# Kernel optimization log

Measured on AMD Instinct MI355X. Metric: run time of the kernel, lower is better.

The kernel has to match this reference:

```python
import jax, jax.numpy as jnp
import numpy as np

B, S, D, H = 2, 2048, 1024, 16
HD = D // H  # 64


def setup_inputs() -> dict:
    key = jax.random.key(0)
    ks = jax.random.split(key, 10)
    q = jax.random.normal(ks[0], (B, S, D), dtype=jnp.float32)
    k = jax.random.normal(ks[1], (B, S, D), dtype=jnp.float32)
    v = jax.random.normal(ks[2], (B, S, D), dtype=jnp.float32)
    # additive mask: 1 where attention is disallowed (causal), broadcast over B,H
    mask = (1.0 - jnp.tril(jnp.ones((S, S), dtype=jnp.float32)))[None, None, :, :]
    sc = 1.0 / np.sqrt(D)
    Wk = jax.random.normal(ks[3], (D, D), dtype=jnp.float32) * sc
    bk = jnp.zeros((D,), dtype=jnp.float32)
    Wv = jax.random.normal(ks[4], (D, D), dtype=jnp.float32) * sc
    bv = jnp.zeros((D,), dtype=jnp.float32)
    Wo = jax.random.normal(ks[5], (D, D), dtype=jnp.float32) * sc
    bo = jnp.zeros((D,), dtype=jnp.float32)
    return {"q": q, "k": k, "v": v, "mask": mask,
            "Wk": Wk, "bk": bk, "Wv": Wv, "bv": bv, "Wo": Wo, "bo": bo}


def _split_heads(x):
    b, s, d = x.shape
    return x.reshape(b, s, H, HD).transpose(0, 2, 1, 3)  # [B,H,S,HD]


def reference(q, k, v, mask, Wk, bk, Wv, bv, Wo, bo):
    # NOTE: source bug reproduced — q is projected with Wk (wq is unused).
    _q = _split_heads(q @ Wk + bk)
    _k = _split_heads(k @ Wk + bk)
    _v = _split_heads(v @ Wv + bv)
    scale = jnp.sqrt(jnp.float32(HD)) + 1e-8
    score = jnp.einsum('bhqd,bhkd->bhqk', _q, _k) / scale
    score = score + mask * (-1e9)
    attn = jax.nn.softmax(score, axis=-1)
    o = jnp.einsum('bhqk,bhkd->bhqd', attn, _v)
    o = o.transpose(0, 2, 1, 3).reshape(q.shape[0], q.shape[1], -1)  # [B,S,D]
    # dropout is identity at inference (training=False)
    return o @ Wo + bo
```

## Files before the change

### kernel.cpp

```cpp
#include <hip/hip_runtime.h>


#define Bn 2
#define Sn 2048
#define Dn 1024
#define Hn 16
#define HDn 64

typedef short bs8 __attribute__((ext_vector_type(8)));
typedef short s4v __attribute__((ext_vector_type(4)));
typedef float f32x4 __attribute__((ext_vector_type(4)));
typedef unsigned int u32;
typedef unsigned int u32x4 __attribute__((ext_vector_type(4)));

__device__ __forceinline__ short f2bf(float f) {
    u32 x = __builtin_bit_cast(u32, f);
    x = x + 0x7fffu + ((x >> 16) & 1u);
    return (short)(x >> 16);
}
__device__ __forceinline__ u32 packbf2(float lo, float hi) {
    u32 a = __builtin_bit_cast(u32, lo);
    u32 b = __builtin_bit_cast(u32, hi);
    a = a + 0x7fffu + ((a >> 16) & 1u);
    b = b + 0x7fffu + ((b >> 16) & 1u);
    return (a >> 16) | (b & 0xffff0000u);
}
__device__ __forceinline__ void gload16(const void* g, void* l) {
    __builtin_amdgcn_global_load_lds(
        (const __attribute__((address_space(1))) u32*)g,
        (__attribute__((address_space(3))) u32*)l, 16, 0, 0);
}

__global__ __launch_bounds__(256) void cvt_qkv(const float* __restrict__ q,
                                               const float* __restrict__ k,
                                               const float* __restrict__ v,
                                               short* __restrict__ out) {
    int z = blockIdx.y;
    const float* in = z == 0 ? q : z == 1 ? k : v;
    short* o = out + (size_t)z * (Bn * Sn * Dn);
    int i = blockIdx.x * 256 + threadIdx.x;
    const f32x4* p = reinterpret_cast<const f32x4*>(in) + (size_t)i * 2;
    f32x4 a = p[0], b = p[1];
    bs8 ov;
    ov[0]=f2bf(a[0]); ov[1]=f2bf(a[1]); ov[2]=f2bf(a[2]); ov[3]=f2bf(a[3]);
    ov[4]=f2bf(b[0]); ov[5]=f2bf(b[1]); ov[6]=f2bf(b[2]); ov[7]=f2bf(b[3]);
    reinterpret_cast<bs8*>(o)[i] = ov;
}

__global__ __launch_bounds__(256) void cvt_w(const float* __restrict__ Wk,
                                             const float* __restrict__ Wv,
                                             const float* __restrict__ Wo,
                                             short* __restrict__ Wt) {
    __shared__ float tile[32][33];
    int z = blockIdx.z;
    const float* W = z == 0 ? Wk : z == 1 ? Wv : Wo;
    short* o = Wt + (size_t)z * Dn * Dn;
    int tx = threadIdx.x & 31;
    int ty = threadIdx.x >> 5;
    int bi = blockIdx.y * 32;
    int bo = blockIdx.x * 32;
    #pragma unroll
    for (int k2 = 0; k2 < 4; k2++)
        tile[ty + k2*8][tx] = W[(size_t)(bi + ty + k2*8) * Dn + bo + tx];
    __syncthreads();
    #pragma unroll
    for (int k2 = 0; k2 < 4; k2++)
        o[(size_t)(bo + ty + k2*8) * Dn + bi + tx] = f2bf(tile[tx][ty + k2*8]);
}

template<int MODE>
__global__ __launch_bounds__(256) void gemm_bt(const short* __restrict__ A,
                                               const short* __restrict__ Bt,
                                               const float* __restrict__ bias,
                                               void* __restrict__ Cout) {
    constexpr int K = Dn, N = Dn;
    __shared__ __align__(16) short As[64][32];
    __shared__ __align__(16) short Bs[128][32];
    int tid = threadIdx.x;
    int m0 = blockIdx.x * 64, n0 = blockIdx.y * 128;
    int w = tid >> 6, lane = tid & 63;
    int wr = (w >> 1) * 32, wc = (w & 1) * 64;
    int fr = lane & 15, fq = lane >> 4;
    f32x4 acc[2][4] = {};
    int srow = tid >> 2, scol = (tid & 3) * 8;
    const short* Ag  = A  + (size_t)(m0 + srow) * K + scol;
    const short* Bg0 = Bt + (size_t)(n0 + srow) * K + scol;
    const short* Bg1 = Bt + (size_t)(n0 + 64 + srow) * K + scol;
    short* AsL  = &As[0][0] + tid * 8;
    short* BsL0 = &Bs[0][0] + tid * 8;
    short* BsL1 = &Bs[0][0] + 2048 + tid * 8;

    for (int k0 = 0; k0 < K; k0 += 32) {
        gload16(Ag + k0, AsL);
        gload16(Bg0 + k0, BsL0);
        gload16(Bg1 + k0, BsL1);
        __syncthreads();
        bs8 af[2], bfv[4];
        #pragma unroll
        for (int i = 0; i < 2; i++)
            af[i] = *reinterpret_cast<const bs8*>(&As[wr + i*16 + fr][fq*8]);
        #pragma unroll
        for (int j = 0; j < 4; j++)
            bfv[j] = *reinterpret_cast<const bs8*>(&Bs[wc + j*16 + fr][fq*8]);
        #pragma unroll
        for (int i = 0; i < 2; i++)
            #pragma unroll
            for (int j = 0; j < 4; j++)
                acc[i][j] = __builtin_amdgcn_mfma_f32_16x16x32_bf16(af[i], bfv[j], acc[i][j], 0, 0, 0);
        __syncthreads();
    }

    #pragma unroll
    for (int j = 0; j < 4; j++) {
        int col = n0 + wc + j*16 + fr;
        float bv = bias[col];
        #pragma unroll
        for (int i = 0; i < 2; i++) {
            int row0 = m0 + wr + i*16 + fq*4;
            #pragma unroll
            for (int r = 0; r < 4; r++) {
                float vv = acc[i][j][r] + bv;
                if (MODE == 0) {
                    ((short*)Cout)[(size_t)(row0 + r) * N + col] = f2bf(vv);
                } else if (MODE == 1) {
                    int t = row0 + r, bb = t >> 11, s = t & (Sn - 1);
                    ((short*)Cout)[(size_t)bb * (Dn*Sn) + (size_t)col * Sn + s] = f2bf(vv);
                } else {
                    ((float*)Cout)[(size_t)(row0 + r) * N + col] = vv;
                }
            }
        }
    }
}

__global__ __launch_bounds__(256) void attn_fwd(const short* __restrict__ Qp,
                                                const short* __restrict__ Kp,
                                                const short* __restrict__ Vt,
                                                short* __restrict__ O) {
    __shared__ __align__(16) char Kb[64 * 128];
    __shared__ __align__(16) char Vb[64 * 128];
    __shared__ __align__(16) short Ot[4][16][72];
    int bh = blockIdx.y, bb = bh >> 4, h = bh & 15;
    int tid = threadIdx.x, w = tid >> 6, lane = tid & 63;
    int fr = lane & 15, fq = lane >> 4;
    int hiA = (fq >> 1) & 1;
    int wloc = w * 16 + fr;
    const float C1 = 0.18033688011112042f;

    int sr = tid >> 2;
    int scB = (tid & 3) * 32;
    int swz = (sr & 7) << 4;
    int wofs0 = sr * 128 + (scB ^ swz);
    int wofs1 = sr * 128 + ((scB + 16) ^ swz);
    const short* Kg = Kp + (size_t)(bb * Sn + sr) * Dn + h * HDn + (tid & 3) * 16;
    const short* Vg = Vt + (size_t)bb * (Dn * Sn) + (size_t)(h * HDn + sr) * Sn + (tid & 3) * 16;

    for (int hf = 0; hf < 2; hf++) {
        int qt = hf ? (31 - (int)blockIdx.x) : (int)blockIdx.x;
        int q0 = qt * 64 + w * 16;
        const short* Qg = Qp + (size_t)(bb * Sn + q0 + fr) * Dn + h * HDn + fq * 8;
        bs8 qf0 = *reinterpret_cast<const bs8*>(Qg);
        bs8 qf1 = *reinterpret_cast<const bs8*>(Qg + 32);
        f32x4 oacc[4] = {};
        float m_run = -3e38f, l_run = 0.f;

        for (int kt = 0; kt <= qt; kt++) {
            int kv0 = kt * 64;
            bs8 k0v = *reinterpret_cast<const bs8*>(Kg + (size_t)kv0 * Dn);
            bs8 k1v = *reinterpret_cast<const bs8*>(Kg + (size_t)kv0 * Dn + 8);
            bs8 v0v = *reinterpret_cast<const bs8*>(Vg + kv0);
            bs8 v1v = *reinterpret_cast<const bs8*>(Vg + kv0 + 8);
            __syncthreads();
            *reinterpret_cast<bs8*>(Kb + wofs0) = k0v;
            *reinterpret_cast<bs8*>(Kb + wofs1) = k1v;
            *reinterpret_cast<bs8*>(Vb + wofs0) = v0v;
            *reinterpret_cast<bs8*>(Vb + wofs1) = v1v;
            __syncthreads();

            float p[4][4];
            #pragma unroll
            for (int n = 0; n < 4; n++) {
                int row = n * 16 + fr;
                int rs = (row & 7) << 4;
                bs8 kf0 = *reinterpret_cast<const bs8*>(Kb + row * 128 + ((fq * 16) ^ rs));
                bs8 kf1 = *reinterpret_cast<const bs8*>(Kb + row * 128 + ((64 + fq * 16) ^ rs));
                f32x4 t = {};
                t = __builtin_amdgcn_mfma_f32_16x16x32_bf16(kf0, qf0, t, 0, 0, 0);
                t = __builtin_amdgcn_mfma_f32_16x16x32_bf16(kf1, qf1, t, 0, 0, 0);
                #pragma unroll
                for (int r = 0; r < 4; r++) p[n][r] = t[r] * C1;
            }
            if (kt == qt) {
                #pragma unroll
                for (int n = 0; n < 4; n++)
                    #pragma unroll
                    for (int r = 0; r < 4; r++)
                        if (n * 16 + fq * 4 + r > wloc) p[n][r] = -2e8f;
            }

            float mloc = p[0][0];
            #pragma unroll
            for (int n = 0; n < 4; n++)
                #pragma unroll
                for (int r = 0; r < 4; r++) mloc = fmaxf(mloc, p[n][r]);
            mloc = fmaxf(mloc, __shfl_xor(mloc, 16));
            mloc = fmaxf(mloc, __shfl_xor(mloc, 32));
            float mn = fmaxf(m_run, mloc);
            float fac = exp2f(m_run - mn);
            m_run = mn;
            float ssum = 0.f;
            #pragma unroll
            for (int n = 0; n < 4; n++)
                #pragma unroll
                for (int r = 0; r < 4; r++) {
                    float e = exp2f(p[n][r] - mn);
                    p[n][r] = e; ssum += e;
                }
            ssum += __shfl_xor(ssum, 16);
            ssum += __shfl_xor(ssum, 32);
            l_run = l_run * fac + ssum;
            #pragma unroll
            for (int n = 0; n < 4; n++) oacc[n] *= fac;

            u32 W0 = packbf2(p[0][0], p[0][1]), W1 = packbf2(p[0][2], p[0][3]);
            u32 W2 = packbf2(p[1][0], p[1][1]), W3 = packbf2(p[1][2], p[1][3]);
            u32 W4 = packbf2(p[2][0], p[2][1]), W5 = packbf2(p[2][2], p[2][3]);
            u32 W6 = packbf2(p[3][0], p[3][1]), W7 = packbf2(p[3][2], p[3][3]);
            u32 sA0 = hiA ? W2 : W0, sA1 = hiA ? W3 : W1;
            u32 sA2 = hiA ? W6 : W4, sA3 = hiA ? W7 : W5;
            u32 sB0 = hiA ? W0 : W2, sB1 = hiA ? W1 : W3;
            u32 sB2 = hiA ? W4 : W6, sB3 = hiA ? W5 : W7;
            u32 x16_0 = (u32)__shfl_xor((int)sA0, 16), x16_1 = (u32)__shfl_xor((int)sA1, 16);
            u32 x16_2 = (u32)__shfl_xor((int)sA2, 16), x16_3 = (u32)__shfl_xor((int)sA3, 16);
            u32 x32_0 = (u32)__shfl_xor((int)sB0, 32), x32_1 = (u32)__shfl_xor((int)sB1, 32);
            u32 x32_2 = (u32)__shfl_xor((int)sB2, 32), x32_3 = (u32)__shfl_xor((int)sB3, 32);
            u32 x48_0 = (u32)__shfl_xor((int)sB0, 48), x48_1 = (u32)__shfl_xor((int)sB1, 48);
            u32 x48_2 = (u32)__shfl_xor((int)sB2, 48), x48_3 = (u32)__shfl_xor((int)sB3, 48);
            u32x4 F0, F1;
            F0[0] = fq==0 ? W0   : fq==1 ? x48_0 : fq==2 ? x32_0 : x16_0;
            F0[1] = fq==0 ? W1   : fq==1 ? x48_1 : fq==2 ? x32_1 : x16_1;
            F0[2] = fq==0 ? x16_0 : fq==1 ? x32_0 : fq==2 ? x48_0 : W2;
            F0[3] = fq==0 ? x16_1 : fq==1 ? x32_1 : fq==2 ? x48_1 : W3;
            F1[0] = fq==0 ? W4   : fq==1 ? x48_2 : fq==2 ? x32_2 : x16_2;
            F1[1] = fq==0 ? W5   : fq==1 ? x48_3 : fq==2 ? x32_3 : x16_3;
            F1[2] = fq==0 ? x16_2 : fq==1 ? x32_2 : fq==2 ? x48_2 : W6;
            F1[3] = fq==0 ? x16_3 : fq==1 ? x32_3 : fq==2 ? x48_3 : W7;
            bs8 pf0 = __builtin_bit_cast(bs8, F0);
            bs8 pf1 = __builtin_bit_cast(bs8, F1);

            #pragma unroll
            for (int n = 0; n < 4; n++) {
                int row = n * 16 + fr;
                int rs = (row & 7) << 4;
                bs8 vf0 = *reinterpret_cast<const bs8*>(Vb + row * 128 + ((fq * 16) ^ rs));
                bs8 vf1 = *reinterpret_cast<const bs8*>(Vb + row * 128 + ((64 + fq * 16) ^ rs));
                oacc[n] = __builtin_amdgcn_mfma_f32_16x16x32_bf16(vf0, pf0, oacc[n], 0, 0, 0);
                oacc[n] = __builtin_amdgcn_mfma_f32_16x16x32_bf16(vf1, pf1, oacc[n], 0, 0, 0);
            }
        }

        float inv = 1.f / l_run;
        #pragma unroll
        for (int n = 0; n < 4; n++) {
            s4v ov;
            #pragma unroll
            for (int r = 0; r < 4; r++) ov[r] = f2bf(oacc[n][r] * inv);
            *reinterpret_cast<s4v*>(&Ot[w][fr][n * 16 + fq * 4]) = ov;
        }
        bs8 o0 = *reinterpret_cast<const bs8*>(&Ot[w][fr][fq * 16]);
        bs8 o1 = *reinterpret_cast<const bs8*>(&Ot[w][fr][fq * 16 + 8]);
        short* Og = O + (size_t)(bb * Sn + q0 + fr) * Dn + h * HDn + fq * 16;
        *reinterpret_cast<bs8*>(Og) = o0;
        *reinterpret_cast<bs8*>(Og + 8) = o1;
    }
}

extern "C" void kernel_launch(void* const* d_in, const int* in_sizes, int n_in,
                              void* d_out, int out_size, void* d_ws, size_t ws_size,
                              hipStream_t stream) {
    const float* q  = (const float*)d_in[0];
    const float* k  = (const float*)d_in[1];
    const float* v  = (const float*)d_in[2];
    const float* Wk = (const float*)d_in[4];
    const float* bk = (const float*)d_in[5];
    const float* Wv = (const float*)d_in[6];
    const float* bv = (const float*)d_in[7];
    const float* Wo = (const float*)d_in[8];
    const float* bo = (const float*)d_in[9];

    char* ws = (char*)d_ws;
    const size_t MB = (size_t)1 << 20;
    short* Wall = (short*)ws;
    short* Wkt  = Wall;
    short* Wvt  = Wall + (1 << 20);
    short* Wot  = Wall + 2 * (1 << 20);
    short* qb   = (short*)(ws + 6*MB);
    short* kb   = (short*)(ws + 14*MB);
    short* vb   = (short*)(ws + 22*MB);
    short* Qp   = (short*)(ws + 30*MB);
    short* Kp   = (short*)(ws + 38*MB);
    short* Vtp  = qb;
    short* Oa   = kb;

    cvt_qkv<<<dim3(2048, 3), dim3(256), 0, stream>>>(q, k, v, qb);
    cvt_w<<<dim3(32, 32, 3), dim3(256), 0, stream>>>(Wk, Wv, Wo, Wall);

    dim3 gg(64, 8);
    gemm_bt<0><<<gg, dim3(256), 0, stream>>>(qb, Wkt, bk, Qp);
    gemm_bt<0><<<gg, dim3(256), 0, stream>>>(kb, Wkt, bk, Kp);
    gemm_bt<1><<<gg, dim3(256), 0, stream>>>(vb, Wvt, bv, Vtp);

    attn_fwd<<<dim3(16, 32), dim3(256), 0, stream>>>(Qp, Kp, Vtp, Oa);

    gemm_bt<2><<<gg, dim3(256), 0, stream>>>(Oa, Wot, bo, d_out);
}
```

Measured before the change: 261.1 us.

## Fuse QKV projections into one launch and restructure attention softmax and P exchange

Replaces three projection GEMM launches with one batched 128x128-tile kernel. The score scale is folded into the Q projection epilogue, and V^T is stored with packed hardware bf16 conversions. Attention now runs one query tile per block on a 32x32 grid instead of pairing tiles, so the grid is larger but the load is less balanced. The P operand is exchanged through LDS instead of many cross-lane shuffles, the max-rescale is skipped lazily unless the max grows by more than 8, and the l reduction is deferred to the end. Together these cut launch overhead, VALU and shuffle work, at the cost of extra LDS traffic and a wider tile that may lower occupancy.

```diff
diff --git a/kernel.cpp b/kernel.cpp
--- a/kernel.cpp
+++ b/kernel.cpp
@@ -8,22 +8,19 @@
 #define HDn 64
 
 typedef short bs8 __attribute__((ext_vector_type(8)));
-typedef short s4v __attribute__((ext_vector_type(4)));
 typedef float f32x4 __attribute__((ext_vector_type(4)));
 typedef unsigned int u32;
-typedef unsigned int u32x4 __attribute__((ext_vector_type(4)));
+typedef unsigned int u32x2 __attribute__((ext_vector_type(2)));
 
 __device__ __forceinline__ short f2bf(float f) {
     u32 x = __builtin_bit_cast(u32, f);
     x = x + 0x7fffu + ((x >> 16) & 1u);
     return (short)(x >> 16);
 }
-__device__ __forceinline__ u32 packbf2(float lo, float hi) {
-    u32 a = __builtin_bit_cast(u32, lo);
-    u32 b = __builtin_bit_cast(u32, hi);
-    a = a + 0x7fffu + ((a >> 16) & 1u);
-    b = b + 0x7fffu + ((b >> 16) & 1u);
-    return (a >> 16) | (b & 0xffff0000u);
+__device__ __forceinline__ u32 cvtpk(float lo, float hi) {
+    u32 r;
+    asm("v_cvt_pk_bf16_f32 %0, %1, %2" : "=v"(r) : "v"(lo), "v"(hi));
+    return r;
 }
 __device__ __forceinline__ void gload16(const void* g, void* l) {
     __builtin_amdgcn_global_load_lds(
@@ -68,11 +65,94 @@
         o[(size_t)(bo + ty + k2*8) * Dn + bi + tx] = f2bf(tile[tx][ty + k2*8]);
 }
 
-template<int MODE>
-__global__ __launch_bounds__(256) void gemm_bt(const short* __restrict__ A,
-                                               const short* __restrict__ Bt,
-                                               const float* __restrict__ bias,
-                                               void* __restrict__ Cout) {
+__global__ __launch_bounds__(256) void proj3(const short* __restrict__ qb,
+                                             const short* __restrict__ kb,
+                                             const short* __restrict__ vb,
+                                             const short* __restrict__ Wall,
+                                             const float* __restrict__ bk,
+                                             const float* __restrict__ bv,
+                                             short* __restrict__ Qp,
+                                             short* __restrict__ Kp,
+                                             short* __restrict__ Vtp) {
+    constexpr int K = Dn;
+    __shared__ __align__(16) short As[128 * 32];
+    __shared__ __align__(16) short Bs[128 * 32];
+    int z = blockIdx.z;
+    const short* A  = z == 0 ? qb : z == 1 ? kb : vb;
+    const short* Bt = z == 2 ? Wall + (1 << 20) : Wall;
+    const float* bias = z == 2 ? bv : bk;
+    int tid = threadIdx.x;
+    int m0 = blockIdx.x * 128, n0 = blockIdx.y * 128;
+    int w = tid >> 6, lane = tid & 63;
+    int wr = (w >> 1) * 64, wc = (w & 1) * 64;
+    int fr = lane & 15, fq = lane >> 4;
+    f32x4 acc[4][4] = {};
+    const short* Ag  = A  + (size_t)(m0 + (tid >> 2)) * K + (tid & 3) * 8;
+    const short* Ag2 = Ag + (size_t)64 * K;
+    const short* Bg  = Bt + (size_t)(n0 + (tid >> 2)) * K + (tid & 3) * 8;
+    const short* Bg2 = Bg + (size_t)64 * K;
+    short* AsL = As + tid * 8;
+    short* BsL = Bs + tid * 8;
+
+    for (int k0 = 0; k0 < K; k0 += 32) {
+        gload16(Ag + k0, AsL);
+        gload16(Ag2 + k0, AsL + 2048);
+        gload16(Bg + k0, BsL);
+        gload16(Bg2 + k0, BsL + 2048);
+        __syncthreads();
+        bs8 af[4], bfv[4];
+        #pragma unroll
+        for (int i = 0; i < 4; i++)
+            af[i] = *reinterpret_cast<const bs8*>(&As[(wr + i*16 + fr) * 32 + fq * 8]);
+        #pragma unroll
+        for (int j = 0; j < 4; j++)
+            bfv[j] = *reinterpret_cast<const bs8*>(&Bs[(wc + j*16 + fr) * 32 + fq * 8]);
+        #pragma unroll
+        for (int i = 0; i < 4; i++)
+            #pragma unroll
+            for (int j = 0; j < 4; j++)
+                acc[i][j] = __builtin_amdgcn_mfma_f32_16x16x32_bf16(af[i], bfv[j], acc[i][j], 0, 0, 0);
+        __syncthreads();
+    }
+
+    if (z == 2) {
+        #pragma unroll
+        for (int j = 0; j < 4; j++) {
+            int col = n0 + wc + j*16 + fr;
+            float bvv = bias[col];
+            #pragma unroll
+            for (int i = 0; i < 4; i++) {
+                int row0 = m0 + wr + i*16 + fq*4;
+                int bb = row0 >> 11, s0 = row0 & (Sn - 1);
+                size_t base = (size_t)bb * (Dn * Sn) + (size_t)col * Sn + s0;
+                u32x2 pv;
+                pv[0] = cvtpk(acc[i][j][0] + bvv, acc[i][j][1] + bvv);
+                pv[1] = cvtpk(acc[i][j][2] + bvv, acc[i][j][3] + bvv);
+                *reinterpret_cast<u32x2*>(&Vtp[base]) = pv;
+            }
+        }
+    } else {
+        float sc = (z == 0) ? 0.18033688011112042f : 1.0f;
+        short* outp = (z == 0) ? Qp : Kp;
+        #pragma unroll
+        for (int j = 0; j < 4; j++) {
+            int col = n0 + wc + j*16 + fr;
+            float bvv = bias[col];
+            #pragma unroll
+            for (int i = 0; i < 4; i++) {
+                int row0 = m0 + wr + i*16 + fq*4;
+                #pragma unroll
+                for (int r = 0; r < 4; r++)
+                    outp[(size_t)(row0 + r) * Dn + col] = f2bf((acc[i][j][r] + bvv) * sc);
+            }
+        }
+    }
+}
+
+__global__ __launch_bounds__(256) void gemm_out(const short* __restrict__ A,
+                                                const short* __restrict__ Bt,
+                                                const float* __restrict__ bias,
+                                                float* __restrict__ Cout) {
     constexpr int K = Dn, N = Dn;
     __shared__ __align__(16) short As[64][32];
     __shared__ __align__(16) short Bs[128][32];
@@ -82,13 +162,12 @@
     int wr = (w >> 1) * 32, wc = (w & 1) * 64;
     int fr = lane & 15, fq = lane >> 4;
     f32x4 acc[2][4] = {};
-    int srow = tid >> 2, scol = (tid & 3) * 8;
-    const short* Ag  = A  + (size_t)(m0 + srow) * K + scol;
-    const short* Bg0 = Bt + (size_t)(n0 + srow) * K + scol;
-    const short* Bg1 = Bt + (size_t)(n0 + 64 + srow) * K + scol;
+    const short* Ag  = A  + (size_t)(m0 + (tid >> 2)) * K + (tid & 3) * 8;
+    const short* Bg0 = Bt + (size_t)(n0 + (tid >> 2)) * K + (tid & 3) * 8;
+    const short* Bg1 = Bg0 + (size_t)64 * K;
     short* AsL  = &As[0][0] + tid * 8;
     short* BsL0 = &Bs[0][0] + tid * 8;
-    short* BsL1 = &Bs[0][0] + 2048 + tid * 8;
+    short* BsL1 = BsL0 + 2048;
 
     for (int k0 = 0; k0 < K; k0 += 32) {
         gload16(Ag + k0, AsL);
@@ -109,7 +188,6 @@
                 acc[i][j] = __builtin_amdgcn_mfma_f32_16x16x32_bf16(af[i], bfv[j], acc[i][j], 0, 0, 0);
         __syncthreads();
     }
-
     #pragma unroll
     for (int j = 0; j < 4; j++) {
         int col = n0 + wc + j*16 + fr;
@@ -118,17 +196,8 @@
         for (int i = 0; i < 2; i++) {
             int row0 = m0 + wr + i*16 + fq*4;
             #pragma unroll
-            for (int r = 0; r < 4; r++) {
-                float vv = acc[i][j][r] + bv;
-                if (MODE == 0) {
-                    ((short*)Cout)[(size_t)(row0 + r) * N + col] = f2bf(vv);
-                } else if (MODE == 1) {
-                    int t = row0 + r, bb = t >> 11, s = t & (Sn - 1);
-                    ((short*)Cout)[(size_t)bb * (Dn*Sn) + (size_t)col * Sn + s] = f2bf(vv);
-                } else {
-                    ((float*)Cout)[(size_t)(row0 + r) * N + col] = vv;
-                }
-            }
+            for (int r = 0; r < 4; r++)
+                Cout[(size_t)(row0 + r) * N + col] = acc[i][j][r] + bv;
         }
     }
 }
@@ -139,140 +208,127 @@
                                                 short* __restrict__ O) {
     __shared__ __align__(16) char Kb[64 * 128];
     __shared__ __align__(16) char Vb[64 * 128];
+    __shared__ __align__(16) u32  Pw[4][16][36];
     __shared__ __align__(16) short Ot[4][16][72];
+    int qt = 31 - (int)blockIdx.x;
     int bh = blockIdx.y, bb = bh >> 4, h = bh & 15;
     int tid = threadIdx.x, w = tid >> 6, lane = tid & 63;
     int fr = lane & 15, fq = lane >> 4;
-    int hiA = (fq >> 1) & 1;
     int wloc = w * 16 + fr;
-    const float C1 = 0.18033688011112042f;
-
-    int sr = tid >> 2;
-    int scB = (tid & 3) * 32;
-    int swz = (sr & 7) << 4;
+    int q0 = qt * 64 + w * 16;
+
+    const short* Qg = Qp + (size_t)(bb * Sn + q0 + fr) * Dn + h * HDn + fq * 8;
+    bs8 qf0 = *reinterpret_cast<const bs8*>(Qg);
+    bs8 qf1 = *reinterpret_cast<const bs8*>(Qg + 32);
+
+    f32x4 oacc[4] = {};
+    float m_run = -3e38f, l_run = 0.f;
+
+    int sr = tid >> 2, scB = (tid & 3) * 32, swz = (sr & 7) << 4;
     int wofs0 = sr * 128 + (scB ^ swz);
     int wofs1 = sr * 128 + ((scB + 16) ^ swz);
     const short* Kg = Kp + (size_t)(bb * Sn + sr) * Dn + h * HDn + (tid & 3) * 16;
     const short* Vg = Vt + (size_t)bb * (Dn * Sn) + (size_t)(h * HDn + sr) * Sn + (tid & 3) * 16;
 
-    for (int hf = 0; hf < 2; hf++) {
-        int qt = hf ? (31 - (int)blockIdx.x) : (int)blockIdx.x;
-        int q0 = qt * 64 + w * 16;
-        const short* Qg = Qp + (size_t)(bb * Sn + q0 + fr) * Dn + h * HDn + fq * 8;
-        bs8 qf0 = *reinterpret_cast<const bs8*>(Qg);
-        bs8 qf1 = *reinterpret_cast<const bs8*>(Qg + 32);
-        f32x4 oacc[4] = {};
-        float m_run = -3e38f, l_run = 0.f;
-
-        for (int kt = 0; kt <= qt; kt++) {
-            int kv0 = kt * 64;
-            bs8 k0v = *reinterpret_cast<const bs8*>(Kg + (size_t)kv0 * Dn);
-            bs8 k1v = *reinterpret_cast<const bs8*>(Kg + (size_t)kv0 * Dn + 8);
-            bs8 v0v = *reinterpret_cast<const bs8*>(Vg + kv0);
-            bs8 v1v = *reinterpret_cast<const bs8*>(Vg + kv0 + 8);
-            __syncthreads();
-            *reinterpret_cast<bs8*>(Kb + wofs0) = k0v;
-            *reinterpret_cast<bs8*>(Kb + wofs1) = k1v;
-            *reinterpret_cast<bs8*>(Vb + wofs0) = v0v;
-            *reinterpret_cast<bs8*>(Vb + wofs1) = v1v;
-            __syncthreads();
-
-            float p[4][4];
-            #pragma unroll
-            for (int n = 0; n < 4; n++) {
-                int row = n * 16 + fr;
-                int rs = (row & 7) << 4;
-                bs8 kf0 = *reinterpret_cast<const bs8*>(Kb + row * 128 + ((fq * 16) ^ rs));
-                bs8 kf1 = *reinterpret_cast<const bs8*>(Kb + row * 128 + ((64 + fq * 16) ^ rs));
-                f32x4 t = {};
-                t = __builtin_amdgcn_mfma_f32_16x16x32_bf16(kf0, qf0, t, 0, 0, 0);
-                t = __builtin_amdgcn_mfma_f32_16x16x32_bf16(kf1, qf1, t, 0, 0, 0);
-                #pragma unroll
-                for (int r = 0; r < 4; r++) p[n][r] = t[r] * C1;
-            }
-            if (kt == qt) {
-                #pragma unroll
-                for (int n = 0; n < 4; n++)
-                    #pragma unroll
-                    for (int r = 0; r < 4; r++)
-                        if (n * 16 + fq * 4 + r > wloc) p[n][r] = -2e8f;
-            }
-
-            float mloc = p[0][0];
+    int rs = (fr & 7) << 4;
+    int rb0 = (fq * 16) ^ rs;
+    int rb1 = (64 + fq * 16) ^ rs;
+    u32* PwL = &Pw[w][fr][0];
+    u32* PwS = PwL + 2 * fq;
+
+    for (int kt = 0; kt <= qt; kt++) {
+        int kv0 = kt * 64;
+        bs8 k0v = *reinterpret_cast<const bs8*>(Kg + (size_t)kv0 * Dn);
+        bs8 k1v = *reinterpret_cast<const bs8*>(Kg + (size_t)kv0 * Dn + 8);
+        bs8 v0v = *reinterpret_cast<const bs8*>(Vg + kv0);
+        bs8 v1v = *reinterpret_cast<const bs8*>(Vg + kv0 + 8);
+        __syncthreads();
+        *reinterpret_cast<bs8*>(Kb + wofs0) = k0v;
+        *reinterpret_cast<bs8*>(Kb + wofs1) = k1v;
+        *reinterpret_cast<bs8*>(Vb + wofs0) = v0v;
+        *reinterpret_cast<bs8*>(Vb + wofs1) = v1v;
+        __syncthreads();
+
+        float p[4][4];
+        #pragma unroll
+        for (int n = 0; n < 4; n++) {
+            const char* Krow = Kb + (n * 16 + fr) * 128;
+            bs8 kf0 = *reinterpret_cast<const bs8*>(Krow + rb0);
+            bs8 kf1 = *reinterpret_cast<const bs8*>(Krow + rb1);
+            f32x4 t = {};
+            t = __builtin_amdgcn_mfma_f32_16x16x32_bf16(kf0, qf0, t, 0, 0, 0);
+            t = __builtin_amdgcn_mfma_f32_16x16x32_bf16(kf1, qf1, t, 0, 0, 0);
+            p[n][0] = t[0]; p[n][1] = t[1]; p[n][2] = t[2]; p[n][3] = t[3];
+        }
+        if (kt == qt) {
             #pragma unroll
             for (int n = 0; n < 4; n++)
                 #pragma unroll
-                for (int r = 0; r < 4; r++) mloc = fmaxf(mloc, p[n][r]);
-            mloc = fmaxf(mloc, __shfl_xor(mloc, 16));
-            mloc = fmaxf(mloc, __shfl_xor(mloc, 32));
+                for (int r = 0; r < 4; r++)
+                    if (n * 16 + fq * 4 + r > wloc) p[n][r] = -1.8e8f;
+        }
+
+        float m01 = fmaxf(fmaxf(p[0][0], p[0][1]), fmaxf(p[0][2], p[0][3]));
+        float m23 = fmaxf(fmaxf(p[1][0], p[1][1]), fmaxf(p[1][2], p[1][3]));
+        float m45 = fmaxf(fmaxf(p[2][0], p[2][1]), fmaxf(p[2][2], p[2][3]));
+        float m67 = fmaxf(fmaxf(p[3][0], p[3][1]), fmaxf(p[3][2], p[3][3]));
+        float mloc = fmaxf(fmaxf(m01, m23), fmaxf(m45, m67));
+        mloc = fmaxf(mloc, __shfl_xor(mloc, 16));
+        mloc = fmaxf(mloc, __shfl_xor(mloc, 32));
+        if (!__all(mloc <= m_run + 8.0f)) {
             float mn = fmaxf(m_run, mloc);
             float fac = exp2f(m_run - mn);
             m_run = mn;
-            float ssum = 0.f;
-            #pragma unroll
-            for (int n = 0; n < 4; n++)
-                #pragma unroll
-                for (int r = 0; r < 4; r++) {
-                    float e = exp2f(p[n][r] - mn);
-                    p[n][r] = e; ssum += e;
-                }
-            ssum += __shfl_xor(ssum, 16);
-            ssum += __shfl_xor(ssum, 32);
-            l_run = l_run * fac + ssum;
-            #pragma unroll
-            for (int n = 0; n < 4; n++) oacc[n] *= fac;
-
-            u32 W0 = packbf2(p[0][0], p[0][1]), W1 = packbf2(p[0][2], p[0][3]);
-            u32 W2 = packbf2(p[1][0], p[1][1]), W3 = packbf2(p[1][2], p[1][3]);
-            u32 W4 = packbf2(p[2][0], p[2][1]), W5 = packbf2(p[2][2], p[2][3]);
-            u32 W6 = packbf2(p[3][0], p[3][1]), W7 = packbf2(p[3][2], p[3][3]);
-            u32 sA0 = hiA ? W2 : W0, sA1 = hiA ? W3 : W1;
-            u32 sA2 = hiA ? W6 : W4, sA3 = hiA ? W7 : W5;
-            u32 sB0 = hiA ? W0 : W2, sB1 = hiA ? W1 : W3;
-            u32 sB2 = hiA ? W4 : W6, sB3 = hiA ? W5 : W7;
-            u32 x16_0 = (u32)__shfl_xor((int)sA0, 16), x16_1 = (u32)__shfl_xor((int)sA1, 16);
-            u32 x16_2 = (u32)__shfl_xor((int)sA2, 16), x16_3 = (u32)__shfl_xor((int)sA3, 16);
-            u32 x32_0 = (u32)__shfl_xor((int)sB0, 32), x32_1 = (u32)__shfl_xor((int)sB1, 32);
-            u32 x32_2 = (u32)__shfl_xor((int)sB2, 32), x32_3 = (u32)__shfl_xor((int)sB3, 32);
-            u32 x48_0 = (u32)__shfl_xor((int)sB0, 48), x48_1 = (u32)__shfl_xor((int)sB1, 48);
-            u32 x48_2 = (u32)__shfl_xor((int)sB2, 48), x48_3 = (u32)__shfl_xor((int)sB3, 48);
-            u32x4 F0, F1;
-            F0[0] = fq==0 ? W0   : fq==1 ? x48_0 : fq==2 ? x32_0 : x16_0;
-            F0[1] = fq==0 ? W1   : fq==1 ? x48_1 : fq==2 ? x32_1 : x16_1;
-            F0[2] = fq==0 ? x16_0 : fq==1 ? x32_0 : fq==2 ? x48_0 : W2;
-            F0[3] = fq==0 ? x16_1 : fq==1 ? x32_1 : fq==2 ? x48_1 : W3;
-            F1[0] = fq==0 ? W4   : fq==1 ? x48_2 : fq==2 ? x32_2 : x16_2;
-            F1[1] = fq==0 ? W5   : fq==1 ? x48_3 : fq==2 ? x32_3 : x16_3;
-            F1[2] = fq==0 ? x16_2 : fq==1 ? x32_2 : fq==2 ? x48_2 : W6;
-            F1[3] = fq==0 ? x16_3 : fq==1 ? x32_3 : fq==2 ? x48_3 : W7;
-            bs8 pf0 = __builtin_bit_cast(bs8, F0);
-            bs8 pf1 = __builtin_bit_cast(bs8, F1);
-
-            #pragma unroll
-            for (int n = 0; n < 4; n++) {
-                int row = n * 16 + fr;
-                int rs = (row & 7) << 4;
-                bs8 vf0 = *reinterpret_cast<const bs8*>(Vb + row * 128 + ((fq * 16) ^ rs));
-                bs8 vf1 = *reinterpret_cast<const bs8*>(Vb + row * 128 + ((64 + fq * 16) ^ rs));
-                oacc[n] = __builtin_amdgcn_mfma_f32_16x16x32_bf16(vf0, pf0, oacc[n], 0, 0, 0);
-                oacc[n] = __builtin_amdgcn_mfma_f32_16x16x32_bf16(vf1, pf1, oacc[n], 0, 0, 0);
+            l_run *= fac;
+            oacc[0] *= fac; oacc[1] *= fac; oacc[2] *= fac; oacc[3] *= fac;
+        }
+        float ssum = 0.f;
+        #pragma unroll
+        for (int n = 0; n < 4; n++)
+            #pragma unroll
+            for (int r = 0; r < 4; r++) {
+                float e = exp2f(p[n][r] - m_run);
+                p[n][r] = e; ssum += e;
             }
-        }
-
-        float inv = 1.f / l_run;
+        l_run += ssum;
+
         #pragma unroll
         for (int n = 0; n < 4; n++) {
-            s4v ov;
-            #pragma unroll
-            for (int r = 0; r < 4; r++) ov[r] = f2bf(oacc[n][r] * inv);
-            *reinterpret_cast<s4v*>(&Ot[w][fr][n * 16 + fq * 4]) = ov;
-        }
-        bs8 o0 = *reinterpret_cast<const bs8*>(&Ot[w][fr][fq * 16]);
-        bs8 o1 = *reinterpret_cast<const bs8*>(&Ot[w][fr][fq * 16 + 8]);
-        short* Og = O + (size_t)(bb * Sn + q0 + fr) * Dn + h * HDn + fq * 16;
-        *reinterpret_cast<bs8*>(Og) = o0;
-        *reinterpret_cast<bs8*>(Og + 8) = o1;
-    }
+            u32x2 pr;
+            pr[0] = cvtpk(p[n][0], p[n][1]);
+            pr[1] = cvtpk(p[n][2], p[n][3]);
+            *reinterpret_cast<u32x2*>(PwS + 8 * n) = pr;
+        }
+        __builtin_amdgcn_wave_barrier();
+        bs8 pf0 = *reinterpret_cast<const bs8*>(PwL + 4 * fq);
+        bs8 pf1 = *reinterpret_cast<const bs8*>(PwL + 16 + 4 * fq);
+
+        #pragma unroll
+        for (int n = 0; n < 4; n++) {
+            const char* Vrow = Vb + (n * 16 + fr) * 128;
+            bs8 vf0 = *reinterpret_cast<const bs8*>(Vrow + rb0);
+            bs8 vf1 = *reinterpret_cast<const bs8*>(Vrow + rb1);
+            oacc[n] = __builtin_amdgcn_mfma_f32_16x16x32_bf16(vf0, pf0, oacc[n], 0, 0, 0);
+            oacc[n] = __builtin_amdgcn_mfma_f32_16x16x32_bf16(vf1, pf1, oacc[n], 0, 0, 0);
+        }
+    }
+
+    l_run += __shfl_xor(l_run, 16);
+    l_run += __shfl_xor(l_run, 32);
+    float inv = 1.f / l_run;
+    #pragma unroll
+    for (int n = 0; n < 4; n++) {
+        u32x2 ov;
+        ov[0] = cvtpk(oacc[n][0] * inv, oacc[n][1] * inv);
+        ov[1] = cvtpk(oacc[n][2] * inv, oacc[n][3] * inv);
+        *reinterpret_cast<u32x2*>(&Ot[w][fr][n * 16 + fq * 4]) = ov;
+    }
+    __builtin_amdgcn_wave_barrier();
+    bs8 o0 = *reinterpret_cast<const bs8*>(&Ot[w][fr][fq * 16]);
+    bs8 o1 = *reinterpret_cast<const bs8*>(&Ot[w][fr][fq * 16 + 8]);
+    short* Og = O + (size_t)(bb * Sn + q0 + fr) * Dn + h * HDn + fq * 16;
+    *reinterpret_cast<bs8*>(Og) = o0;
+    *reinterpret_cast<bs8*>(Og + 8) = o1;
 }
 
 extern "C" void kernel_launch(void* const* d_in, const int* in_sizes, int n_in,
@@ -291,26 +347,21 @@
     char* ws = (char*)d_ws;
     const size_t MB = (size_t)1 << 20;
     short* Wall = (short*)ws;
-    short* Wkt  = Wall;
-    short* Wvt  = Wall + (1 << 20);
     short* Wot  = Wall + 2 * (1 << 20);
     short* qb   = (short*)(ws + 6*MB);
     short* kb   = (short*)(ws + 14*MB);
     short* vb   = (short*)(ws + 22*MB);
     short* Qp   = (short*)(ws + 30*MB);
     short* Kp   = (short*)(ws + 38*MB);
-    short* Vtp  = qb;
-    short* Oa   = kb;
+    short* Vtp  = (short*)(ws + 46*MB);
+    short* Oa   = qb;
 
     cvt_qkv<<<dim3(2048, 3), dim3(256), 0, stream>>>(q, k, v, qb);
     cvt_w<<<dim3(32, 32, 3), dim3(256), 0, stream>>>(Wk, Wv, Wo, Wall);
 
-    dim3 gg(64, 8);
-    gemm_bt<0><<<gg, dim3(256), 0, stream>>>(qb, Wkt, bk, Qp);
-    gemm_bt<0><<<gg, dim3(256), 0, stream>>>(kb, Wkt, bk, Kp);
-    gemm_bt<1><<<gg, dim3(256), 0, stream>>>(vb, Wvt, bv, Vtp);
-
-    attn_fwd<<<dim3(16, 32), dim3(256), 0, stream>>>(Qp, Kp, Vtp, Oa);
-
-    gemm_bt<2><<<gg, dim3(256), 0, stream>>>(Oa, Wot, bo, d_out);
-}
+    proj3<<<dim3(32, 8, 3), dim3(256), 0, stream>>>(qb, kb, vb, Wall, bk, bv, Qp, Kp, Vtp);
+
+    attn_fwd<<<dim3(32, 32), dim3(256), 0, stream>>>(Qp, Kp, Vtp, Oa);
+
+    gemm_out<<<dim3(64, 8), dim3(256), 0, stream>>>(Oa, Wot, bo, (float*)d_out);
+}
```

Result: no change. 261.0 us (-0.0%).
